# Performance work log

Measured on AMD Instinct MI355X. Metric: run time of the kernel, lower is better.

The kernel has to match this reference:

```python
import jax, jax.numpy as jnp
import numpy as np


def setup_inputs() -> dict:
    key = jax.random.key(0)
    k1, k2, k3 = jax.random.split(key, 3)
    B, F, D = 32, 4096, 256
    x = jax.random.normal(k1, (B, F, D), dtype=jnp.float32)
    mask = jax.random.randint(k2, (B, 1, F), 0, 2).astype(bool)
    query = 0.02 * jax.random.normal(k3, (1, D), dtype=jnp.float32)
    return {"x": x, "mask": mask, "query": query}


def reference(x, mask, query):
    # x: (B, F, D), mask: (B, 1, F) bool (True = ignore), query: (1, D)
    m = mask[..., 0, :]                                  # (B, F)
    scores = jnp.einsum("bfd,d->bf", x, query[0])        # (B, F)
    scores = jnp.where(m, -jnp.inf, scores)
    w = jax.nn.softmax(scores, axis=-1)                  # (B, F)
    w = jnp.where(m, 0.0, w)
    out = jnp.einsum("bf,bfd->bd", w, x)                 # (B, D)
    return out
```

## Files before the change

kernel.cpp:

```cpp
#include <hip/hip_runtime.h>
#include <math.h>

#define B 32
#define F 4096
#define D 256


__device__ __forceinline__ int mask_at(const void* mask, int mode, int row) {
    if (mode == 0) return ((const unsigned char*)mask)[row];
    if (mode == 1) return ((const int*)mask)[row];
    if (mode == 2) return ((const int*)mask)[row << 1];
    if (mode == 3) return ((const unsigned int*)mask)[row] != 0u;
    return ((const unsigned short*)mask)[row] != 0;
}

__global__ __launch_bounds__(256) void k_fused(const float* __restrict__ x,
                                               const void* __restrict__ mask,
                                               const float* __restrict__ q,
                                               float* __restrict__ acc,
                                               float* __restrict__ lsum_g
                                               ) {
    const int t    = threadIdx.x;
    const int lane = t & 63;
    const int w    = t >> 6;
    const int b    = blockIdx.x >> 6;
    const int f0   = (blockIdx.x & 63) << 6;

    __shared__ int s_mode;
    if (w == 0) {
        const unsigned int m = ((const unsigned int*)mask)[lane];
        const unsigned int lo = m & 0xFFFFu, hi = m >> 16;
        const bool w01  = (m <= 1u);
        const bool odnz = (lane & 1) && (m != 0u);
        const bool f32k = (m == 0u) || (m == 0x3F800000u);
        const bool b16k = (lo == 0u || lo == 0x3F80u) && (hi == 0u || hi == 0x3F80u);
        const bool all01  = __ballot(w01)  == ~0ull;
        const bool anyodd = __ballot(odnz) != 0ull;
        const bool allf32 = __ballot(f32k) == ~0ull;
        const bool allb16 = __ballot(b16k) == ~0ull;
        if (lane == 0)
            s_mode = all01 ? (anyodd ? 1 : 2) : (allf32 ? 3 : (allb16 ? 4 : 0));
    }
    __syncthreads();
    const int mode = s_mode;

    const float4 qv = ((const float4*)q)[lane];
    float4 a = make_float4(0.f, 0.f, 0.f, 0.f);
    float  lw = 0.f;

#pragma unroll 4
    for (int i = 0; i < 16; ++i) {
        const int row = (b << 12) + f0 + (i << 2) + w;
        if (mask_at(mask, mode, row)) continue;
        const float4 xv = *(const float4*)(x + (((size_t)row) << 8) + (lane << 2));
        float s = qv.x * xv.x + qv.y * xv.y + qv.z * xv.z + qv.w * xv.w;
#pragma unroll
        for (int o = 32; o; o >>= 1) s += __shfl_xor(s, o, 64);
        const float wgt = expf(s);
        a.x += wgt * xv.x;  a.y += wgt * xv.y;
        a.z += wgt * xv.z;  a.w += wgt * xv.w;
        lw  += wgt;
    }

    __shared__ float sacc[4][D];
    __shared__ float sl[4];
    *(float4*)&sacc[w][lane << 2] = a;
    if (lane == 0) sl[w] = lw;
    __syncthreads();
    const float v = sacc[0][t] + sacc[1][t] + sacc[2][t] + sacc[3][t];
    atomicAdd(&acc[(b << 8) + t], v);
    if (t == 0) atomicAdd(&lsum_g[b], sl[0] + sl[1] + sl[2] + sl[3]);
}

__global__ __launch_bounds__(256) void k_final(const float* __restrict__ acc,
                                               const float* __restrict__ lsum_g,
                                               float* __restrict__ out) {
    const int b = blockIdx.x, t = threadIdx.x;
    const float l = lsum_g[b];
    out[(b << 8) + t] = (l > 0.f) ? acc[(b << 8) + t] / l : 0.f;
}

extern "C" void kernel_launch(void* const* d_in, const int* in_sizes, int n_in,
                              void* d_out, int out_size, void* d_ws, size_t ws_size,
                              hipStream_t stream) {
    const float* x    = (const float*)d_in[0];
    const void*  mask = d_in[1];
    const float* q    = (const float*)d_in[2];
    float*       out  = (float*)d_out;

    float* acc  = (float*)d_ws;
    float* lsum = acc + (size_t)B * D;

    hipMemsetAsync(acc, 0, ((size_t)B * D + B) * sizeof(float), stream);
    k_fused<<<B * (F / 64), 256, 0, stream>>>(x, mask, q, acc, lsum);
    k_final<<<B,            256, 0, stream>>>(acc, lsum, out);
}
```

Measured before the change: 200.5 us.

## Replace global atomics with per-chunk partials and deterministic final reduction

Each block now writes its 256-wide partial accumulator and weight sum to a per-block workspace slot instead of issuing atomicAdds to a shared per-batch accumulator. The final kernel sums the 64 chunk partials per batch and reduces the weight sums with a wavefront shuffle. This removes the memset launch and the atomic contention. Every wavefront now computes the mask-mode detection itself, so the shared-memory broadcast and one __syncthreads go away. In exchange there are extra workspace writes (about 2 MB of partials) and a heavier final kernel.

```diff
diff --git a/kernel.cpp b/kernel.cpp
--- a/kernel.cpp
+++ b/kernel.cpp
@@ -4,6 +4,7 @@
 #define B 32
 #define F 4096
 #define D 256
+#define CHUNKS 64
 
 
 __device__ __forceinline__ int mask_at(const void* mask, int mode, int row) {
@@ -17,32 +18,22 @@
 __global__ __launch_bounds__(256) void k_fused(const float* __restrict__ x,
                                                const void* __restrict__ mask,
                                                const float* __restrict__ q,
-                                               float* __restrict__ acc,
-                                               float* __restrict__ lsum_g
-                                               ) {
+                                               float* __restrict__ pacc,
+                                               float* __restrict__ pl) {
     const int t    = threadIdx.x;
     const int lane = t & 63;
     const int w    = t >> 6;
     const int b    = blockIdx.x >> 6;
     const int f0   = (blockIdx.x & 63) << 6;
 
-    __shared__ int s_mode;
-    if (w == 0) {
-        const unsigned int m = ((const unsigned int*)mask)[lane];
-        const unsigned int lo = m & 0xFFFFu, hi = m >> 16;
-        const bool w01  = (m <= 1u);
-        const bool odnz = (lane & 1) && (m != 0u);
-        const bool f32k = (m == 0u) || (m == 0x3F800000u);
-        const bool b16k = (lo == 0u || lo == 0x3F80u) && (hi == 0u || hi == 0x3F80u);
-        const bool all01  = __ballot(w01)  == ~0ull;
-        const bool anyodd = __ballot(odnz) != 0ull;
-        const bool allf32 = __ballot(f32k) == ~0ull;
-        const bool allb16 = __ballot(b16k) == ~0ull;
-        if (lane == 0)
-            s_mode = all01 ? (anyodd ? 1 : 2) : (allf32 ? 3 : (allb16 ? 4 : 0));
-    }
-    __syncthreads();
-    const int mode = s_mode;
+    const unsigned int mword = ((const unsigned int*)mask)[lane];
+    const unsigned int lo = mword & 0xFFFFu, hi = mword >> 16;
+    const bool all01  = __ballot(mword <= 1u) == ~0ull;
+    const bool anyodd = __ballot((lane & 1) && mword != 0u) != 0ull;
+    const bool allf32 = __ballot(mword == 0u || mword == 0x3F800000u) == ~0ull;
+    const bool allb16 = __ballot((lo == 0u || lo == 0x3F80u) &&
+                                 (hi == 0u || hi == 0x3F80u)) == ~0ull;
+    const int mode = all01 ? (anyodd ? 1 : 2) : (allf32 ? 3 : (allb16 ? 4 : 0));
 
     const float4 qv = ((const float4*)q)[lane];
     float4 a = make_float4(0.f, 0.f, 0.f, 0.f);
@@ -67,17 +58,31 @@
     *(float4*)&sacc[w][lane << 2] = a;
     if (lane == 0) sl[w] = lw;
     __syncthreads();
-    const float v = sacc[0][t] + sacc[1][t] + sacc[2][t] + sacc[3][t];
-    atomicAdd(&acc[(b << 8) + t], v);
-    if (t == 0) atomicAdd(&lsum_g[b], sl[0] + sl[1] + sl[2] + sl[3]);
+    pacc[(blockIdx.x << 8) + t] = sacc[0][t] + sacc[1][t] + sacc[2][t] + sacc[3][t];
+    if (t == 0) pl[blockIdx.x] = sl[0] + sl[1] + sl[2] + sl[3];
 }
 
-__global__ __launch_bounds__(256) void k_final(const float* __restrict__ acc,
-                                               const float* __restrict__ lsum_g,
+__global__ __launch_bounds__(256) void k_final(const float* __restrict__ pacc,
+                                               const float* __restrict__ pl,
                                                float* __restrict__ out) {
     const int b = blockIdx.x, t = threadIdx.x;
-    const float l = lsum_g[b];
-    out[(b << 8) + t] = (l > 0.f) ? acc[(b << 8) + t] / l : 0.f;
+    const int lane = t & 63, w = t >> 6;
+
+    float a = 0.f;
+    const float* p = pacc + ((size_t)b << 14) + t;
+#pragma unroll 8
+    for (int c = 0; c < CHUNKS; ++c) a += p[c << 8];
+
+    __shared__ float sl_tot;
+    if (w == 0) {
+        float l = pl[(b << 6) + lane];
+#pragma unroll
+        for (int o = 32; o; o >>= 1) l += __shfl_xor(l, o, 64);
+        if (lane == 0) sl_tot = l;
+    }
+    __syncthreads();
+    const float l = sl_tot;
+    out[(b << 8) + t] = (l > 0.f) ? a / l : 0.f;
 }
 
 extern "C" void kernel_launch(void* const* d_in, const int* in_sizes, int n_in,
@@ -88,10 +93,9 @@
     const float* q    = (const float*)d_in[2];
     float*       out  = (float*)d_out;
 
-    float* acc  = (float*)d_ws;
-    float* lsum = acc + (size_t)B * D;
+    float* pacc = (float*)d_ws;
+    float* pl   = pacc + (size_t)B * CHUNKS * D;
 
-    hipMemsetAsync(acc, 0, ((size_t)B * D + B) * sizeof(float), stream);
-    k_fused<<<B * (F / 64), 256, 0, stream>>>(x, mask, q, acc, lsum);
-    k_final<<<B,            256, 0, stream>>>(acc, lsum, out);
+    k_fused<<<B * CHUNKS, 256, 0, stream>>>(x, mask, q, pacc, pl);
+    k_final<<<B,          256, 0, stream>>>(pacc, pl, out);
 }
```

Measured after the change: 190.3 us. 5.1% less time.
